# Optimization experiments

Hardware: AMD Instinct MI355X
Metric: run time of the kernel (lower is better)

Reference implementation:

```python
import jax, jax.numpy as jnp
import numpy as np

NUM_ENTITY = 100000
NUM_TYPE = 5000
DIM = 128
BATCH = 512
MARGIN = 2.0


def setup_inputs() -> dict:
    key = jax.random.key(0)
    k1, k2, k3 = jax.random.split(key, 3)
    x_batch = jax.random.randint(k1, (BATCH,), 0, NUM_ENTITY)
    # xavier_uniform-style init for embedding tables
    lim_e = float(np.sqrt(6.0 / (NUM_ENTITY + DIM)))
    lim_t = float(np.sqrt(6.0 / (NUM_TYPE + DIM)))
    ent_table = jax.random.uniform(k2, (NUM_ENTITY, DIM), minval=-lim_e, maxval=lim_e, dtype=jnp.float32)
    type_table = jax.random.uniform(k3, (NUM_TYPE, DIM), minval=-lim_t, maxval=lim_t, dtype=jnp.float32)
    # padding_idx=0 rows are zero in torch Embedding
    ent_table = ent_table.at[0].set(0.0)
    type_table = type_table.at[0].set(0.0)
    return {"ent_table": ent_table, "type_table": type_table, "x_batch": x_batch}


def reference(ent_table, type_table, x_batch):
    # [B, D] entity embedding lookup
    e = ent_table[x_batch]
    # L1 distance from each entity to every type embedding: [B, T]
    dist = jnp.sum(jnp.abs(e[:, None, :] - type_table[None, :, :]), axis=2)
    return jax.nn.sigmoid(MARGIN - dist)
```

## Files before the change

### kernel.cpp

```cpp
#include <hip/hip_runtime.h>
#include <math.h>

#define NUM_ENTITY 100000
#define NUM_TYPE   5000
#define DIM        128
#define BATCH      512
#define MARGIN     2.0f

#define TG 64
#define BG 8
#define TSTRIDE 68

typedef _Float16 half_t;
typedef half_t half2_t __attribute__((ext_vector_type(2)));

__device__ __forceinline__ uint32_t pk2(float x, float y) {
    return __builtin_bit_cast(uint32_t, __builtin_amdgcn_cvt_pkrtz(x, y));
}

__device__ __forceinline__ float absdot(uint32_t eu, uint32_t tu, float acc) {
    const half2_t ones = {(half_t)1.0f, (half_t)1.0f};
    half2_t d = __builtin_bit_cast(half2_t, eu) - __builtin_bit_cast(half2_t, tu);
    const uint32_t du = __builtin_bit_cast(uint32_t, d) & 0x7fff7fffu;
#if __has_builtin(__builtin_amdgcn_fdot2)
    return __builtin_amdgcn_fdot2(__builtin_bit_cast(half2_t, du), ones, acc, false);
#else
    half2_t a = __builtin_bit_cast(half2_t, du);
    return acc + (float)a[0] + (float)a[1];
#endif
}

__global__ __launch_bounds__(64, 1) void l1dist_sigmoid_kernel(
    const float* __restrict__ ent,
    const float* __restrict__ typ,
    const int*   __restrict__ xb,
    float*       __restrict__ out)
{
    __shared__ uint32_t tL[TG * TSTRIDE];
    __shared__ uint32_t eL[BG * 64];

    const int l  = threadIdx.x;
    const int t0 = blockIdx.x * TG;
    const int b0 = blockIdx.y * BG;

#pragma unroll
    for (int s = 0; s < 4; ++s) {
        const int g   = l + 64 * s;
        const int row = g >> 5;
        const int c4  = g & 31;
        const int er  = xb[b0 + row];
        const float4 v = *(const float4*)&ent[er * DIM + c4 * 4];
        uint2 w;
        w.x = pk2(v.x, v.y);
        w.y = pk2(v.z, v.w);
        *(uint2*)&eL[row * 64 + c4 * 2] = w;
    }

#pragma unroll 8
    for (int s = 0; s < 32; ++s) {
        const int g   = l + 64 * s;
        const int row = g >> 5;
        const int c4  = g & 31;
        const int tr  = min(t0 + row, NUM_TYPE - 1);
        const float4 v = *(const float4*)&typ[tr * DIM + c4 * 4];
        uint2 w;
        w.x = pk2(v.x, v.y);
        w.y = pk2(v.z, v.w);
        *(uint2*)&tL[row * TSTRIDE + c4 * 2] = w;
    }

    __syncthreads();

    uint4 tf[16];
#pragma unroll
    for (int c = 0; c < 16; ++c)
        tf[c] = *(const uint4*)&tL[l * TSTRIDE + c * 4];

    const bool valid = (t0 + l) < NUM_TYPE;

#pragma unroll 1
    for (int i = 0; i < BG; ++i) {
        float acc = 0.0f;
#pragma unroll
        for (int c = 0; c < 16; ++c) {
            const uint4 ev = *(const uint4*)&eL[i * 64 + c * 4];
            acc = absdot(ev.x, tf[c].x, acc);
            acc = absdot(ev.y, tf[c].y, acc);
            acc = absdot(ev.z, tf[c].z, acc);
            acc = absdot(ev.w, tf[c].w, acc);
        }
        if (valid) {
            const float x = MARGIN - acc;
            out[(b0 + i) * NUM_TYPE + t0 + l] = 1.0f / (1.0f + __expf(-x));
        }
    }
}

extern "C" void kernel_launch(void* const* d_in, const int* in_sizes, int n_in,
                              void* d_out, int out_size, void* d_ws, size_t ws_size,
                              hipStream_t stream) {
    const float* ent = (const float*)d_in[0];
    const float* typ = (const float*)d_in[1];
    const int*   xb  = (const int*)d_in[2];
    float*       out = (float*)d_out;

    dim3 grid((NUM_TYPE + TG - 1) / TG, BATCH / BG);
    dim3 block(64);
    l1dist_sigmoid_kernel<<<grid, block, 0, stream>>>(ent, typ, xb, out);
}
```

Baseline: 30.50 us.

## Share each type tile across four wavefronts covering 32 batch rows

Blocks grow from one wavefront to four (256 threads). All four waves share one staged 64-row type tile, and each wave handles its own 8 batch rows, so a block covers 32 batch rows instead of 8. This cuts the number of times each type row is reloaded and converted from global memory by four, and shrinks the grid by the same factor. The inner dimension loop moves from full unroll to unroll 4. That makes the per-thread register array `tf[c]` dynamically indexed, which risks scratch spills or indexed register moves.

```diff
diff --git a/kernel.cpp b/kernel.cpp
--- a/kernel.cpp
+++ b/kernel.cpp
@@ -8,6 +8,7 @@
 #define MARGIN     2.0f
 
 #define TG 64
+#define BB 32
 #define BG 8
 #define TSTRIDE 68
 
@@ -30,43 +31,45 @@
 #endif
 }
 
-__global__ __launch_bounds__(64, 1) void l1dist_sigmoid_kernel(
+__global__ __launch_bounds__(256, 2) void l1dist_sigmoid_kernel(
     const float* __restrict__ ent,
     const float* __restrict__ typ,
     const int*   __restrict__ xb,
     float*       __restrict__ out)
 {
     __shared__ uint32_t tL[TG * TSTRIDE];
-    __shared__ uint32_t eL[BG * 64];
+    __shared__ uint32_t eL[BB * 64];
 
-    const int l  = threadIdx.x;
-    const int t0 = blockIdx.x * TG;
-    const int b0 = blockIdx.y * BG;
+    const int tid = threadIdx.x;
+    const int l   = tid & 63;
+    const int w   = tid >> 6;
+    const int t0  = blockIdx.x * TG;
+    const int b0  = blockIdx.y * BB;
 
 #pragma unroll
     for (int s = 0; s < 4; ++s) {
-        const int g   = l + 64 * s;
+        const int g   = tid + 256 * s;
         const int row = g >> 5;
         const int c4  = g & 31;
         const int er  = xb[b0 + row];
         const float4 v = *(const float4*)&ent[er * DIM + c4 * 4];
-        uint2 w;
-        w.x = pk2(v.x, v.y);
-        w.y = pk2(v.z, v.w);
-        *(uint2*)&eL[row * 64 + c4 * 2] = w;
+        uint2 pw;
+        pw.x = pk2(v.x, v.y);
+        pw.y = pk2(v.z, v.w);
+        *(uint2*)&eL[row * 64 + c4 * 2] = pw;
     }
 
-#pragma unroll 8
-    for (int s = 0; s < 32; ++s) {
-        const int g   = l + 64 * s;
+#pragma unroll
+    for (int s = 0; s < 8; ++s) {
+        const int g   = tid + 256 * s;
         const int row = g >> 5;
         const int c4  = g & 31;
         const int tr  = min(t0 + row, NUM_TYPE - 1);
         const float4 v = *(const float4*)&typ[tr * DIM + c4 * 4];
-        uint2 w;
-        w.x = pk2(v.x, v.y);
-        w.y = pk2(v.z, v.w);
-        *(uint2*)&tL[row * TSTRIDE + c4 * 2] = w;
+        uint2 pw;
+        pw.x = pk2(v.x, v.y);
+        pw.y = pk2(v.z, v.w);
+        *(uint2*)&tL[row * TSTRIDE + c4 * 2] = pw;
     }
 
     __syncthreads();
@@ -77,13 +80,14 @@
         tf[c] = *(const uint4*)&tL[l * TSTRIDE + c * 4];
 
     const bool valid = (t0 + l) < NUM_TYPE;
+    const int  wb    = w * BG;
 
 #pragma unroll 1
     for (int i = 0; i < BG; ++i) {
         float acc = 0.0f;
-#pragma unroll
+#pragma unroll 4
         for (int c = 0; c < 16; ++c) {
-            const uint4 ev = *(const uint4*)&eL[i * 64 + c * 4];
+            const uint4 ev = *(const uint4*)&eL[(wb + i) * 64 + c * 4];
             acc = absdot(ev.x, tf[c].x, acc);
             acc = absdot(ev.y, tf[c].y, acc);
             acc = absdot(ev.z, tf[c].z, acc);
@@ -91,7 +95,7 @@
         }
         if (valid) {
             const float x = MARGIN - acc;
-            out[(b0 + i) * NUM_TYPE + t0 + l] = 1.0f / (1.0f + __expf(-x));
+            out[(b0 + wb + i) * NUM_TYPE + t0 + l] = 1.0f / (1.0f + __expf(-x));
         }
     }
 }
@@ -104,7 +108,7 @@
     const int*   xb  = (const int*)d_in[2];
     float*       out = (float*)d_out;
 
-    dim3 grid((NUM_TYPE + TG - 1) / TG, BATCH / BG);
-    dim3 block(64);
+    dim3 grid((NUM_TYPE + TG - 1) / TG, BATCH / BB);
+    dim3 block(256);
     l1dist_sigmoid_kernel<<<grid, block, 0, stream>>>(ent, typ, xb, out);
 }
```

After: 99.33 us. 3.26x slower.
